# Kernel optimization log

Hardware: AMD Instinct MI355X
Metric: run time of the kernel (lower is better)

## Reference

```python
import jax, jax.numpy as jnp
import numpy as np

DIM = 512
HEADS = 16
WH, WW = 8, 8
N = WH * WW
B_ = 1024
NW = 64
CPB_HID = 512


def setup_inputs() -> dict:
    key = jax.random.key(0)
    ks = jax.random.split(key, 10)
    x = jax.random.normal(ks[0], (B_, N, DIM), dtype=jnp.float32)
    # 0 / -100 shifted-window style additive mask (finite stand-in for -inf)
    mask = jnp.where(jax.random.uniform(ks[1], (NW, N, N)) < 0.1, -100.0, 0.0).astype(jnp.float32)
    qkv_w = jax.random.normal(ks[2], (DIM, 3 * DIM), dtype=jnp.float32) * 0.02
    q_bias = jnp.zeros((DIM,), jnp.float32)
    v_bias = jnp.zeros((DIM,), jnp.float32)
    logit_scale = jnp.log(10.0 * jnp.ones((1, HEADS, 1, 1), jnp.float32))
    cpb_w1 = jax.random.normal(ks[3], (2, CPB_HID), dtype=jnp.float32) * 0.02
    cpb_b1 = jnp.zeros((CPB_HID,), jnp.float32)
    cpb_w2 = jax.random.normal(ks[4], (CPB_HID, HEADS), dtype=jnp.float32) * 0.02
    proj_w = jax.random.normal(ks[5], (DIM, DIM), dtype=jnp.float32) * 0.02
    proj_b = jnp.zeros((DIM,), jnp.float32)
    return dict(x=x, mask=mask, qkv_w=qkv_w, q_bias=q_bias, v_bias=v_bias,
                logit_scale=logit_scale, cpb_w1=cpb_w1, cpb_b1=cpb_b1,
                cpb_w2=cpb_w2, proj_w=proj_w, proj_b=proj_b)


def _coords_table():
    # continuous relative coords table, normalized/log-scaled as in Swin-V2
    rel_h = jnp.arange(-(WH - 1), WH, dtype=jnp.float32)
    rel_w = jnp.arange(-(WW - 1), WW, dtype=jnp.float32)
    t = jnp.stack(jnp.meshgrid(rel_h, rel_w), axis=-1)  # (2Ww-1, 2Wh-1, 2)
    t = t / jnp.array([WH - 1, WW - 1], dtype=jnp.float32)
    t = t * 8.0
    t = jnp.sign(t) * jnp.log2(jnp.abs(t) + 1.0) / jnp.log2(jnp.float32(8.0))
    return t.reshape(-1, 2)  # ((2Wh-1)*(2Ww-1), 2)


def _rel_pos_index():
    ch = jnp.arange(WH)
    cw = jnp.arange(WW)
    coords = jnp.stack(jnp.meshgrid(ch, cw))          # (2, Ww, Wh), xy indexing
    cf = coords.reshape(2, -1)                        # (2, N)
    rel = cf[:, :, None] - cf[:, None, :]             # (2, N, N)
    ry = (rel[0] + WH - 1) * (2 * WW - 1)
    rx = rel[1] + WW - 1
    return (ry + rx).reshape(-1)                      # (N*N,) int


def reference(x, mask, qkv_w, q_bias, v_bias, logit_scale, cpb_w1, cpb_b1, cpb_w2, proj_w, proj_b):
    Bw, n, C = x.shape
    hd = C // HEADS
    # qkv with bias = [q_bias, 0, v_bias]
    qkv_bias = jnp.concatenate([q_bias, jnp.zeros_like(v_bias), v_bias])
    qkv = x @ qkv_w + qkv_bias                        # (B_, N, 3C)
    qkv = qkv.reshape(Bw, n, 3, HEADS, hd).transpose(2, 0, 3, 1, 4)
    q, k, v = qkv[0], qkv[1], qkv[2]                  # (B_, H, N, hd)
    # cosine attention
    qn = q / jnp.linalg.norm(q, axis=-1, keepdims=True)
    kn = k / jnp.linalg.norm(k, axis=-1, keepdims=True)
    attn = jnp.einsum('bhnd,bhmd->bhnm', qn, kn)
    scale = jnp.exp(jnp.minimum(logit_scale, jnp.log(jnp.float32(100.0))))
    attn = attn * scale
    # continuous position bias: MLP(table) then gather by relative index
    table = _coords_table()
    bias_table = jax.nn.relu(table @ cpb_w1 + cpb_b1) @ cpb_w2   # (T, H)
    rpb = bias_table[_rel_pos_index()].reshape(n, n, HEADS).transpose(2, 0, 1)
    rpb = 16.0 * jax.nn.sigmoid(rpb)
    attn = attn + rpb[None]                           # (B_, H, N, N)
    # shifted-window mask
    nW = mask.shape[0]
    attn = attn.reshape(Bw // nW, nW, HEADS, n, n) + mask[None, :, None]
    attn = attn.reshape(Bw, HEADS, n, n)
    attn = jax.nn.softmax(attn, axis=-1)
    out = jnp.einsum('bhnm,bhmd->bhnd', attn, v)
    out = out.transpose(0, 2, 1, 3).reshape(Bw, n, C)
    return out @ proj_w + proj_b
```

## Files before the change

### kernel.cpp

```cpp
#include <hip/hip_runtime.h>
#include <cstdint>

typedef unsigned short u16;
typedef float    f32x4  __attribute__((ext_vector_type(4)));
typedef __bf16   bf16x8 __attribute__((ext_vector_type(8)));
typedef unsigned int u32x4 __attribute__((ext_vector_type(4)));

#define DIMC   512
#define HEADS  16
#define NTOK   64
#define BWIN   1024
#define HD     32
#define QKV_ONE (1024u*16u*64u*32u)

__device__ __forceinline__ u16 f2bf(float x) {
  unsigned u = __float_as_uint(x);
  u += 0x7FFFu + ((u >> 16) & 1u);
  return (u16)(u >> 16);
}
__device__ __forceinline__ float bf2f(u16 h) {
  return __uint_as_float(((unsigned)h) << 16);
}
__device__ __forceinline__ void gld16(const u16* g, u16* l) {
  __builtin_amdgcn_global_load_lds((const __attribute__((address_space(1))) void*)g,
                                   (__attribute__((address_space(3))) void*)l, 16, 0, 0);
}

__global__ void cpb_kernel(const float* __restrict__ w1, const float* __restrict__ b1,
                           const float* __restrict__ w2, float* __restrict__ table) {
  int t  = blockIdx.x;
  int ti = t / 15, tj = t % 15;
  float v0 = (float)(tj - 7) * (8.0f / 7.0f);
  float v1 = (float)(ti - 7) * (8.0f / 7.0f);
  float c0 = copysignf(log2f(fabsf(v0) + 1.0f) / 3.0f, v0);
  float c1 = copysignf(log2f(fabsf(v1) + 1.0f) / 3.0f, v1);
  float acc[HEADS];
#pragma unroll
  for (int h = 0; h < HEADS; ++h) acc[h] = 0.f;
  for (int k = threadIdx.x; k < 512; k += 64) {
    float hid = fmaxf(c0 * w1[k] + c1 * w1[512 + k] + b1[k], 0.0f);
#pragma unroll
    for (int h = 0; h < HEADS; ++h) acc[h] += hid * w2[k * HEADS + h];
  }
#pragma unroll
  for (int off = 32; off >= 1; off >>= 1) {
#pragma unroll
    for (int h = 0; h < HEADS; ++h) acc[h] += __shfl_xor(acc[h], off, 64);
  }
  if (threadIdx.x == 0) {
#pragma unroll
    for (int h = 0; h < HEADS; ++h) table[t * HEADS + h] = acc[h];
  }
}

__global__ void cbias_kernel(const float* __restrict__ table, const float* __restrict__ mask,
                             float* __restrict__ cbias) {
  int wh = blockIdx.x; int w = wh >> 4, h = wh & 15;
  const float* mrow = mask + (size_t)w * 4096;
  float* crow = cbias + (size_t)wh * 4096;
  for (int e = threadIdx.x; e < 4096; e += blockDim.x) {
    int i = e >> 6, j = e & 63;
    int dh = (i & 7) - (j & 7);
    int dw = (i >> 3) - (j >> 3);
    int idx = (dh + 7) * 15 + (dw + 7);
    float r = table[idx * HEADS + h];
    float rpb = 16.0f / (1.0f + __expf(-r));
    crow[e] = rpb + mrow[e];
  }
}

__global__ void cast_x_kernel(const float* __restrict__ src, u16* __restrict__ dst, int n8) {
  int i = blockIdx.x * blockDim.x + threadIdx.x;
  if (i >= n8) return;
  const f32x4* s4 = (const f32x4*)src;
  f32x4 a = s4[(size_t)2 * i], b = s4[(size_t)2 * i + 1];
  u16 o[8];
#pragma unroll
  for (int j = 0; j < 4; ++j) { o[j] = f2bf(a[j]); o[4 + j] = f2bf(b[j]); }
  *(u32x4*)(dst + (size_t)i * 8) = *(const u32x4*)o;
}

__global__ void tcast_kernel(const float* __restrict__ w, u16* __restrict__ wt, int K, int N) {
  int i = blockIdx.x * blockDim.x + threadIdx.x;
  if (i >= K * N) return;
  int n = i / K, k = i % K;
  wt[i] = f2bf(w[(size_t)k * N + n]);
}

template <int EPI>
__global__ __launch_bounds__(256, 2) void gemm_kernel(
    const u16* __restrict__ A, const u16* __restrict__ Bt,
    const float* __restrict__ bias0, const float* __restrict__ bias1,
    void* __restrict__ outp, int M, int N, int K) {
  constexpr int BM = 128, BN = 128, BK = 32;
  __shared__ u16 As[BM * BK];
  __shared__ u16 Bs[BN * BK];
  const int nb = N / BN;
  const int m0 = (blockIdx.x / nb) * BM;
  const int n0 = (blockIdx.x % nb) * BN;
  const int tid = threadIdx.x;
  const int lane = tid & 63, wid = tid >> 6;
  const int wm = wid >> 1, wn = wid & 1;
  const int quad = lane >> 4, li = lane & 15;
  const int lr = lane >> 2, lc = (lane & 3) * 8;

  const f32x4 z = {0.f, 0.f, 0.f, 0.f};
  f32x4 acc[4][4];
#pragma unroll
  for (int i = 0; i < 4; ++i)
#pragma unroll
    for (int j = 0; j < 4; ++j) acc[i][j] = z;

  const u16* ga = A  + (size_t)(m0 + wid * 32 + lr) * K + lc;
  const u16* gb = Bt + (size_t)(n0 + wid * 32 + lr) * K + lc;
  u16* la0 = &As[(wid * 32) * BK];
  u16* la1 = &As[(wid * 32 + 16) * BK];
  u16* lb0 = &Bs[(wid * 32) * BK];
  u16* lb1 = &Bs[(wid * 32 + 16) * BK];

  for (int k0 = 0; k0 < K; k0 += BK) {
    gld16(ga, la0); gld16(ga + (size_t)16 * K, la1);
    gld16(gb, lb0); gld16(gb + (size_t)16 * K, lb1);
    ga += BK; gb += BK;
    __syncthreads();
    bf16x8 af[4], bfr[4];
#pragma unroll
    for (int mt = 0; mt < 4; ++mt)
      af[mt] = *(const bf16x8*)(As + (wm * 64 + mt * 16 + li) * BK + quad * 8);
#pragma unroll
    for (int nt = 0; nt < 4; ++nt)
      bfr[nt] = *(const bf16x8*)(Bs + (wn * 64 + nt * 16 + li) * BK + quad * 8);
#pragma unroll
    for (int mt = 0; mt < 4; ++mt)
#pragma unroll
      for (int nt = 0; nt < 4; ++nt)
        acc[mt][nt] = __builtin_amdgcn_mfma_f32_16x16x32_bf16(af[mt], bfr[nt], acc[mt][nt], 0, 0, 0);
    __syncthreads();
  }

  if (EPI == 0) {
    u16* qkvp = (u16*)outp;
#pragma unroll
    for (int nt = 0; nt < 4; ++nt) {
      int n = n0 + wn * 64 + nt * 16 + li;
      float bv = (n < 512) ? bias0[n] : ((n < 1024) ? 0.f : bias1[n - 1024]);
      int three = n >> 9, h = (n >> 5) & 15, d = n & 31;
#pragma unroll
      for (int mt = 0; mt < 4; ++mt) {
#pragma unroll
        for (int r = 0; r < 4; ++r) {
          int m = m0 + wm * 64 + mt * 16 + quad * 4 + r;
          int b = m >> 6, t = m & 63;
          size_t dst = (size_t)three * QKV_ONE + (((size_t)(b * 16 + h) * 64 + t) * 32) + d;
          qkvp[dst] = f2bf(acc[mt][nt][r] + bv);
        }
      }
    }
  } else {
    float* op = (float*)outp;
#pragma unroll
    for (int nt = 0; nt < 4; ++nt) {
      int n = n0 + wn * 64 + nt * 16 + li;
      float bv = bias0[n];
#pragma unroll
      for (int mt = 0; mt < 4; ++mt) {
#pragma unroll
        for (int r = 0; r < 4; ++r) {
          int m = m0 + wm * 64 + mt * 16 + quad * 4 + r;
          op[(size_t)m * N + n] = acc[mt][nt][r] + bv;
        }
      }
    }
  }
}

__global__ __launch_bounds__(256, 2) void attn_kernel(
    const u16* __restrict__ qkv, const float* __restrict__ cbias,
    const float* __restrict__ lsc, u16* __restrict__ attn_out) {
  __shared__ u16 qs[64 * 40], ks[64 * 40];
  __shared__ u16 vt[32 * 72];
  __shared__ u16 ps[64 * 72];
  __shared__ float invq[64], invk[64];
  const int bid = blockIdx.x;
  const int b = bid >> 4, h = bid & 15;
  const int tid = threadIdx.x, lane = tid & 63, wid = tid >> 6;
  const int quad = lane >> 4, li = lane & 15;
  const size_t base = (size_t)(b * HEADS + h) * (64 * 32);
  const u16* qp = qkv + base;
  const u16* kp = qp + (size_t)QKV_ONE;
  const u16* vp = qp + (size_t)2 * QKV_ONE;
  {
    int r = tid >> 2, c = (tid & 3) * 8;
    u32x4 q4 = *(const u32x4*)(qp + r * 32 + c);
    u32x4 k4 = *(const u32x4*)(kp + r * 32 + c);
    u32x4 v4 = *(const u32x4*)(vp + r * 32 + c);
    *(u32x4*)(qs + r * 40 + c) = q4;
    *(u32x4*)(ks + r * 40 + c) = k4;
    u16 tmp[8];
    *(u32x4*)tmp = v4;
#pragma unroll
    for (int j = 0; j < 8; ++j) vt[(c + j) * 72 + r] = tmp[j];
  }
  __syncthreads();
  if (tid < 128) {
    int r = tid & 63;
    const u16* src = (tid < 64) ? qs : ks;
    float s = 0.f;
#pragma unroll
    for (int d = 0; d < 32; ++d) { float x = bf2f(src[r * 40 + d]); s += x * x; }
    float inv = rsqrtf(s);
    if (tid < 64) invq[r] = inv; else invk[r] = inv;
  }
  __syncthreads();

  const float scale = __expf(fminf(lsc[h], 4.6051701859880914f));

  const f32x4 z = {0.f, 0.f, 0.f, 0.f};
  f32x4 sacc[4] = {z, z, z, z};
  bf16x8 qa = *(const bf16x8*)(qs + (wid * 16 + li) * 40 + quad * 8);
#pragma unroll
  for (int nt = 0; nt < 4; ++nt) {
    bf16x8 kb = *(const bf16x8*)(ks + (nt * 16 + li) * 40 + quad * 8);
    sacc[nt] = __builtin_amdgcn_mfma_f32_16x16x32_bf16(qa, kb, sacc[nt], 0, 0, 0);
  }
  const float* cb = cbias + ((size_t)(b & 63) * HEADS + h) * 4096;
  float lg[4][4];
#pragma unroll
  for (int nt = 0; nt < 4; ++nt) {
#pragma unroll
    for (int r = 0; r < 4; ++r) {
      int row = wid * 16 + quad * 4 + r;
      int col = nt * 16 + li;
      lg[nt][r] = sacc[nt][r] * invq[row] * invk[col] * scale + cb[row * 64 + col];
    }
  }
#pragma unroll
  for (int r = 0; r < 4; ++r) {
    float mx = fmaxf(fmaxf(lg[0][r], lg[1][r]), fmaxf(lg[2][r], lg[3][r]));
#pragma unroll
    for (int off = 1; off < 16; off <<= 1) mx = fmaxf(mx, __shfl_xor(mx, off, 64));
    float e[4], s = 0.f;
#pragma unroll
    for (int nt = 0; nt < 4; ++nt) { e[nt] = __expf(lg[nt][r] - mx); s += e[nt]; }
#pragma unroll
    for (int off = 1; off < 16; off <<= 1) s += __shfl_xor(s, off, 64);
    float rs = 1.0f / s;
    int row = wid * 16 + quad * 4 + r;
#pragma unroll
    for (int nt = 0; nt < 4; ++nt) ps[row * 72 + nt * 16 + li] = f2bf(e[nt] * rs);
  }
  f32x4 oacc[2] = {z, z};
#pragma unroll
  for (int kc = 0; kc < 2; ++kc) {
    bf16x8 pa = *(const bf16x8*)(ps + (wid * 16 + li) * 72 + kc * 32 + quad * 8);
#pragma unroll
    for (int nt = 0; nt < 2; ++nt) {
      bf16x8 vb = *(const bf16x8*)(vt + (nt * 16 + li) * 72 + kc * 32 + quad * 8);
      oacc[nt] = __builtin_amdgcn_mfma_f32_16x16x32_bf16(pa, vb, oacc[nt], 0, 0, 0);
    }
  }
  u16* op = attn_out + ((size_t)b * 64) * DIMC + h * HD;
#pragma unroll
  for (int nt = 0; nt < 2; ++nt) {
#pragma unroll
    for (int r = 0; r < 4; ++r) {
      int row = wid * 16 + quad * 4 + r;
      op[(size_t)row * DIMC + nt * 16 + li] = f2bf(oacc[nt][r]);
    }
  }
}

extern "C" void kernel_launch(void* const* d_in, const int* in_sizes, int n_in,
                              void* d_out, int out_size, void* d_ws, size_t ws_size,
                              hipStream_t stream) {
  const float* x    = (const float*)d_in[0];
  const float* mask = (const float*)d_in[1];
  const float* qkvw = (const float*)d_in[2];
  const float* qb   = (const float*)d_in[3];
  const float* vb   = (const float*)d_in[4];
  const float* lsc  = (const float*)d_in[5];
  const float* w1   = (const float*)d_in[6];
  const float* b1   = (const float*)d_in[7];
  const float* w2   = (const float*)d_in[8];
  const float* pw   = (const float*)d_in[9];
  const float* pb   = (const float*)d_in[10];
  float* out = (float*)d_out;

  char* ws = (char*)d_ws;
  u16*   x_bf    = (u16*)(ws);
  u16*   qkv_bf  = (u16*)(ws + 67108864);
  u16*   attn_o  = x_bf;
  u16*   wqkv_t  = (u16*)(ws + 268435456);
  u16*   wproj_t = (u16*)(ws + 270008320);
  float* table   = (float*)(ws + 270532608);
  float* cbias   = (float*)(ws + 270548992);

  cpb_kernel<<<225, 64, 0, stream>>>(w1, b1, w2, table);
  cbias_kernel<<<1024, 256, 0, stream>>>(table, mask, cbias);
  cast_x_kernel<<<16384, 256, 0, stream>>>(x, x_bf, 65536 * 512 / 8);
  tcast_kernel<<<3072, 256, 0, stream>>>(qkvw, wqkv_t, 512, 1536);
  tcast_kernel<<<1024, 256, 0, stream>>>(pw, wproj_t, 512, 512);
  gemm_kernel<0><<<512 * 12, 256, 0, stream>>>(x_bf, wqkv_t, qb, vb, qkv_bf, 65536, 1536, 512);
  attn_kernel<<<16384, 256, 0, stream>>>(qkv_bf, cbias, lsc, attn_o);
  gemm_kernel<1><<<512 * 4, 256, 0, stream>>>(attn_o, wproj_t, pb, nullptr, out, 65536, 512, 512);
}
```

Baseline: 545.2 us.

## Rewrite GEMMs as 256x256-tile, 8-wave, 4-stage pipelined swizzled LDS kernels

Measured after the change: 549.7 us. About the same (+0.8%).

```diff
diff --git a/kernel.cpp b/kernel.cpp
--- a/kernel.cpp
+++ b/kernel.cpp
@@ -87,56 +87,85 @@
   wt[i] = f2bf(w[(size_t)k * N + n]);
 }
 
+#define STAGE(slot) do {                                           \
+    u16* _sb = lds + (slot) * 16384;                               \
+    gld16(ga, _sb + aW);                                           \
+    gld16(ga + (size_t)16 * K, _sb + aW + 16 * 32);                \
+    gld16(gb, _sb + 8192 + aW);                                    \
+    gld16(gb + (size_t)16 * K, _sb + 8192 + aW + 16 * 32);         \
+    ga += 32; gb += 32; } while (0)
+
+#define COMPUTE(slot) do {                                         \
+    const u16* _cb = lds + (slot) * 16384;                         \
+    bf16x8 afr[8], bfr[4];                                         \
+    _Pragma("unroll")                                              \
+    for (int mt = 0; mt < 8; ++mt) afr[mt] = *(const bf16x8*)(_cb + aoff[mt]); \
+    _Pragma("unroll")                                              \
+    for (int nt = 0; nt < 4; ++nt) bfr[nt] = *(const bf16x8*)(_cb + boff[nt]); \
+    __builtin_amdgcn_s_setprio(1);                                 \
+    _Pragma("unroll")                                              \
+    for (int mt = 0; mt < 8; ++mt)                                 \
+      _Pragma("unroll")                                            \
+      for (int nt = 0; nt < 4; ++nt)                               \
+        acc[mt][nt] = __builtin_amdgcn_mfma_f32_16x16x32_bf16(afr[mt], bfr[nt], acc[mt][nt], 0, 0, 0); \
+    __builtin_amdgcn_s_setprio(0); } while (0)
+
+#define WAITB(n) do {                                              \
+    asm volatile("s_waitcnt vmcnt(" #n ")" ::: "memory");          \
+    __builtin_amdgcn_s_barrier();                                  \
+    asm volatile("" ::: "memory"); } while (0)
+
 template <int EPI>
-__global__ __launch_bounds__(256, 2) void gemm_kernel(
+__global__ __launch_bounds__(512, 2) void gemm8_kernel(
     const u16* __restrict__ A, const u16* __restrict__ Bt,
     const float* __restrict__ bias0, const float* __restrict__ bias1,
     void* __restrict__ outp, int M, int N, int K) {
-  constexpr int BM = 128, BN = 128, BK = 32;
-  __shared__ u16 As[BM * BK];
-  __shared__ u16 Bs[BN * BK];
-  const int nb = N / BN;
-  const int m0 = (blockIdx.x / nb) * BM;
-  const int n0 = (blockIdx.x % nb) * BN;
-  const int tid = threadIdx.x;
-  const int lane = tid & 63, wid = tid >> 6;
-  const int wm = wid >> 1, wn = wid & 1;
+  extern __shared__ u16 lds[];
+  const int nb = N >> 8;
+  const int cpx = gridDim.x >> 3;
+  const int bid = blockIdx.x;
+  const int wg = (bid & 7) * cpx + (bid >> 3);
+  const int m0 = (wg / nb) << 8;
+  const int n0 = (wg % nb) << 8;
+  const int tid = threadIdx.x, lane = tid & 63, wid = tid >> 6;
+  const int wm = wid >> 2, wn = wid & 3;
   const int quad = lane >> 4, li = lane & 15;
-  const int lr = lane >> 2, lc = (lane & 3) * 8;
+
+  const int srow = lane >> 2;
+  const int scol = ((lane & 3) ^ (srow & 3)) << 3;
+  const u16* ga = A  + (size_t)(m0 + wid * 32 + srow) * K + scol;
+  const u16* gb = Bt + (size_t)(n0 + wid * 32 + srow) * K + scol;
+  const int aW = wid * 32 * 32;
+
+  int aoff[8], boff[4];
+#pragma unroll
+  for (int mt = 0; mt < 8; ++mt)
+    aoff[mt] = (wm * 128 + mt * 16 + li) * 32 + ((quad ^ (li & 3)) << 3);
+#pragma unroll
+  for (int nt = 0; nt < 4; ++nt)
+    boff[nt] = 8192 + (wn * 64 + nt * 16 + li) * 32 + ((quad ^ (li & 3)) << 3);
 
   const f32x4 z = {0.f, 0.f, 0.f, 0.f};
-  f32x4 acc[4][4];
-#pragma unroll
-  for (int i = 0; i < 4; ++i)
+  f32x4 acc[8][4];
+#pragma unroll
+  for (int i = 0; i < 8; ++i)
 #pragma unroll
     for (int j = 0; j < 4; ++j) acc[i][j] = z;
 
-  const u16* ga = A  + (size_t)(m0 + wid * 32 + lr) * K + lc;
-  const u16* gb = Bt + (size_t)(n0 + wid * 32 + lr) * K + lc;
-  u16* la0 = &As[(wid * 32) * BK];
-  u16* la1 = &As[(wid * 32 + 16) * BK];
-  u16* lb0 = &Bs[(wid * 32) * BK];
-  u16* lb1 = &Bs[(wid * 32 + 16) * BK];
-
-  for (int k0 = 0; k0 < K; k0 += BK) {
-    gld16(ga, la0); gld16(ga + (size_t)16 * K, la1);
-    gld16(gb, lb0); gld16(gb + (size_t)16 * K, lb1);
-    ga += BK; gb += BK;
-    __syncthreads();
-    bf16x8 af[4], bfr[4];
-#pragma unroll
-    for (int mt = 0; mt < 4; ++mt)
-      af[mt] = *(const bf16x8*)(As + (wm * 64 + mt * 16 + li) * BK + quad * 8);
-#pragma unroll
-    for (int nt = 0; nt < 4; ++nt)
-      bfr[nt] = *(const bf16x8*)(Bs + (wn * 64 + nt * 16 + li) * BK + quad * 8);
-#pragma unroll
-    for (int mt = 0; mt < 4; ++mt)
-#pragma unroll
-      for (int nt = 0; nt < 4; ++nt)
-        acc[mt][nt] = __builtin_amdgcn_mfma_f32_16x16x32_bf16(af[mt], bfr[nt], acc[mt][nt], 0, 0, 0);
-    __syncthreads();
-  }
+  STAGE(0); STAGE(1); STAGE(2);
+  WAITB(8);
+
+  const int KT = K >> 5;
+  for (int t = 0; t < KT - 3; ++t) {
+    STAGE((t + 3) & 3);
+    COMPUTE(t & 3);
+    WAITB(8);
+  }
+  COMPUTE((KT - 3) & 3);
+  WAITB(4);
+  COMPUTE((KT - 2) & 3);
+  WAITB(0);
+  COMPUTE((KT - 1) & 3);
 
   if (EPI == 0) {
     u16* qkvp = (u16*)outp;
@@ -146,12 +175,12 @@
       float bv = (n < 512) ? bias0[n] : ((n < 1024) ? 0.f : bias1[n - 1024]);
       int three = n >> 9, h = (n >> 5) & 15, d = n & 31;
 #pragma unroll
-      for (int mt = 0; mt < 4; ++mt) {
+      for (int mt = 0; mt < 8; ++mt) {
 #pragma unroll
         for (int r = 0; r < 4; ++r) {
-          int m = m0 + wm * 64 + mt * 16 + quad * 4 + r;
-          int b = m >> 6, t = m & 63;
-          size_t dst = (size_t)three * QKV_ONE + (((size_t)(b * 16 + h) * 64 + t) * 32) + d;
+          int m = m0 + wm * 128 + mt * 16 + quad * 4 + r;
+          int b = m >> 6, tk = m & 63;
+          size_t dst = (size_t)three * QKV_ONE + (((size_t)(b * 16 + h) * 64 + tk) * 32) + d;
           qkvp[dst] = f2bf(acc[mt][nt][r] + bv);
         }
       }
@@ -163,10 +192,10 @@
       int n = n0 + wn * 64 + nt * 16 + li;
       float bv = bias0[n];
 #pragma unroll
-      for (int mt = 0; mt < 4; ++mt) {
+      for (int mt = 0; mt < 8; ++mt) {
 #pragma unroll
         for (int r = 0; r < 4; ++r) {
-          int m = m0 + wm * 64 + mt * 16 + quad * 4 + r;
+          int m = m0 + wm * 128 + mt * 16 + quad * 4 + r;
           op[(size_t)m * N + n] = acc[mt][nt][r] + bv;
         }
       }
@@ -295,12 +324,21 @@
   float* table   = (float*)(ws + 270532608);
   float* cbias   = (float*)(ws + 270548992);
 
+  static int inited = 0;
+  if (!inited) {
+    hipFuncSetAttribute(reinterpret_cast<const void*>(&gemm8_kernel<0>),
+                        hipFuncAttributeMaxDynamicSharedMemorySize, 131072);
+    hipFuncSetAttribute(reinterpret_cast<const void*>(&gemm8_kernel<1>),
+                        hipFuncAttributeMaxDynamicSharedMemorySize, 131072);
+    inited = 1;
+  }
+
   cpb_kernel<<<225, 64, 0, stream>>>(w1, b1, w2, table);
   cbias_kernel<<<1024, 256, 0, stream>>>(table, mask, cbias);
   cast_x_kernel<<<16384, 256, 0, stream>>>(x, x_bf, 65536 * 512 / 8);
   tcast_kernel<<<3072, 256, 0, stream>>>(qkvw, wqkv_t, 512, 1536);
   tcast_kernel<<<1024, 256, 0, stream>>>(pw, wproj_t, 512, 512);
-  gemm_kernel<0><<<512 * 12, 256, 0, stream>>>(x_bf, wqkv_t, qb, vb, qkv_bf, 65536, 1536, 512);
+  gemm8_kernel<0><<<1536, 512, 131072, stream>>>(x_bf, wqkv_t, qb, vb, qkv_bf, 65536, 1536, 512);
   attn_kernel<<<16384, 256, 0, stream>>>(qkv_bf, cbias, lsc, attn_o);
-  gemm_kernel<1><<<512 * 4, 256, 0, stream>>>(attn_o, wproj_t, pb, nullptr, out, 65536, 512, 512);
-}
+  gemm8_kernel<1><<<512, 512, 131072, stream>>>(attn_o, wproj_t, pb, nullptr, out, 65536, 512, 512);
+}
```
